# Optimization experiments

Measured on AMD Instinct MI355X. Metric: run time of the kernel, lower is better.

Reference implementation:

```python
import jax, jax.numpy as jnp
import numpy as np

EPS = 1e-5  # torch BatchNorm1d / LayerNorm default eps
B, S, CTX, C, H = 64, 31, 2048, 512, 8  # S must be num_particles+1 = 31
DH = C // H


def layernorm(x, g, b):
    mu = x.mean(-1, keepdims=True)
    var = x.var(-1, keepdims=True)
    return (x - mu) / jnp.sqrt(var + EPS) * g + b


def setup_inputs() -> dict:
    key = jax.random.key(0)
    ks = jax.random.split(key, 16)
    w = lambda k, shape: jax.random.normal(k, shape, jnp.float32) * 0.02
    return {
        "queries": jax.random.normal(ks[0], (B, S, C), jnp.float32),
        "contexts": jax.random.normal(ks[1], (B, CTX, C), jnp.float32),
        # SelfAttention params (BatchNorm1d(C) in training mode, q/k/v no bias, out with bias)
        "sa_bn_g": jnp.ones((C,), jnp.float32),
        "sa_bn_b": jnp.zeros((C,), jnp.float32),
        "sa_q_w": w(ks[2], (C, C)),
        "sa_k_w": w(ks[3], (C, C)),
        "sa_v_w": w(ks[4], (C, C)),
        "sa_out_w": w(ks[5], (C, C)),
        "sa_out_b": jnp.zeros((C,), jnp.float32),
        "sa_pre_g": jnp.ones((S * S,), jnp.float32),  # BatchNorm1d(961) on energy
        "sa_pre_b": jnp.zeros((S * S,), jnp.float32),
        # Cross Attention params (LayerNorm on queries, q/k/v no bias, out with bias)
        "ca_ln_g": jnp.ones((C,), jnp.float32),
        "ca_ln_b": jnp.zeros((C,), jnp.float32),
        "ca_q_w": w(ks[6], (C, C)),
        "ca_k_w": w(ks[7], (C, C)),
        "ca_v_w": w(ks[8], (C, C)),
        "ca_out_w": w(ks[9], (C, C)),
        "ca_out_b": jnp.zeros((C,), jnp.float32),
        # FFN: LN -> SiLU -> Linear(C,2C,no bias) -> LN -> SiLU -> Linear(2C,C,no bias)
        "ff_ln1_g": jnp.ones((C,), jnp.float32),
        "ff_ln1_b": jnp.zeros((C,), jnp.float32),
        "ff_w1": w(ks[10], (2 * C, C)),
        "ff_ln2_g": jnp.ones((2 * C,), jnp.float32),
        "ff_ln2_b": jnp.zeros((2 * C,), jnp.float32),
        "ff_w2": w(ks[11], (C, 2 * C)),
    }


def reference(queries, contexts, sa_bn_g, sa_bn_b, sa_q_w, sa_k_w, sa_v_w,
              sa_out_w, sa_out_b, sa_pre_g, sa_pre_b, ca_ln_g, ca_ln_b,
              ca_q_w, ca_k_w, ca_v_w, ca_out_w, ca_out_b, ff_ln1_g, ff_ln1_b,
              ff_w1, ff_ln2_g, ff_ln2_b, ff_w2):
    scale = jnp.sqrt(jnp.asarray(C, queries.dtype))

    # ---- SelfAttention (normalization='Batch', training-mode batch stats) ----
    mu = queries.mean(axis=(0, 1))            # per-channel over (B, S)
    var = queries.var(axis=(0, 1))
    xn = (queries - mu) / jnp.sqrt(var + EPS) * sa_bn_g + sa_bn_b
    q = jnp.einsum('bsc,oc->bso', xn, sa_q_w).reshape(B, S, H, DH)
    k = jnp.einsum('bsc,oc->bso', xn, sa_k_w).reshape(B, S, H, DH)
    v = jnp.einsum('bsc,oc->bso', xn, sa_v_w).reshape(B, S, H, DH)
    energy = jnp.einsum('nqhc,nkhc->nhqk', q, k)          # (B,H,S,S)
    # pre-softmax BatchNorm1d over channels = flattened (q,k) positions, batch dims = (B, H)
    e = energy.reshape(B, H, S * S)                        # (B,H,S*S)
    mu2 = e.mean(axis=(0, 1))
    var2 = e.var(axis=(0, 1))
    en = (e - mu2) / jnp.sqrt(var2 + EPS) * sa_pre_g + sa_pre_b
    energy_post = en.reshape(B, H, S, S)
    attn = jax.nn.softmax(energy_post / scale, axis=-1)
    o = jnp.einsum('nhql,nlhc->nqhc', attn, v).reshape(B, S, C)
    o = jnp.einsum('bsc,oc->bso', o, sa_out_w) + sa_out_b
    x_sa = o + queries                                     # residual

    # ---- Cross Attention (LayerNorm on queries pre-projection) ----
    qn = layernorm(x_sa, ca_ln_g, ca_ln_b)
    q2 = jnp.einsum('bsc,oc->bso', qn, ca_q_w).reshape(B, S, H, DH)
    k2 = jnp.einsum('btc,oc->bto', contexts, ca_k_w).reshape(B, CTX, H, DH)
    v2 = jnp.einsum('btc,oc->bto', contexts, ca_v_w).reshape(B, CTX, H, DH)
    energy2 = jnp.einsum('nqhc,nkhc->nhqk', q2, k2)        # (B,H,S,CTX)
    attn2 = jax.nn.softmax(energy2 / scale, axis=-1)
    o2 = jnp.einsum('nhql,nlhc->nqhc', attn2, v2).reshape(B, S, C)
    o2 = jnp.einsum('bsc,oc->bso', o2, ca_out_w) + ca_out_b
    x_ca = o2 + x_sa                                       # residual (queries_pre)

    # ---- FFN: LN -> SiLU -> Linear -> LN -> SiLU -> Linear, + residual ----
    h = jax.nn.silu(layernorm(x_ca, ff_ln1_g, ff_ln1_b))
    h = jnp.einsum('bsc,oc->bso', h, ff_w1)                # (B,S,2C)
    h = jax.nn.silu(layernorm(h, ff_ln2_g, ff_ln2_b))
    h = jnp.einsum('bsc,oc->bso', h, ff_w2)                # (B,S,C)
    out = x_ca + h                                         # dropout p=0.0 -> identity
    return out, energy2
```

## Files before the change

kernel.cpp:

```cpp
#include <hip/hip_runtime.h>
#include <hip/hip_bf16.h>
#include <cstdint>
#include <cstddef>

using u16 = unsigned short;
typedef short short8 __attribute__((ext_vector_type(8)));
typedef short short4v __attribute__((ext_vector_type(4)));
typedef float f32x4  __attribute__((ext_vector_type(4)));

#define DEV static __device__ __forceinline__

DEV float b2f(u16 u){ union{ unsigned i; float f; } v; v.i = ((unsigned)u)<<16; return v.f; }
DEV u16 f2b(float f){
  unsigned i = __builtin_bit_cast(unsigned, f);
  unsigned r = (i + 0x7FFFu + ((i>>16)&1u)) >> 16;
  return (u16)r;
}
DEV f32x4 mfma16(short8 a, short8 b, f32x4 c){
  return __builtin_amdgcn_mfma_f32_16x16x32_bf16(a, b, c, 0, 0, 0);
}

constexpr int Bn=64, Sn=31, Tn=2048, Cn=512, Hn=8;
constexpr int Rn=Bn*Sn;
constexpr int BHn=Bn*Hn;
constexpr int HRn=Hn*Sn;
constexpr float EPSf=1e-5f;
constexpr float INV_SCALE=0.04419417382415922f;

__global__ void k_badorder(float* out){
  if(threadIdx.x==0) out[0]=2000.f;
}

struct Src8 { const float* p[8]; };
__global__ __launch_bounds__(256) void k_cvtbn(Src8 s, u16* __restrict__ dst,
    const float* __restrict__ q, float* __restrict__ ps, float* __restrict__ psq){
  int bid=blockIdx.x;
  if(bid<1280){
    int i = bid*256 + threadIdx.x;
    int seg, j=i;
    if(j>=196608){ if(j>=262144){seg=7;j-=262144;} else {seg=6;j-=196608;} }
    else { seg=j>>15; j&=32767; }
    const float* src=s.p[seg];
    f32x4 a=*(const f32x4*)&src[(size_t)j*8];
    f32x4 b=*(const f32x4*)&src[(size_t)j*8+4];
    short8 o;
    #pragma unroll
    for(int qq=0;qq<4;++qq){ o[qq]=(short)f2b(a[qq]); o[4+qq]=(short)f2b(b[qq]); }
    *(short8*)&dst[(size_t)i*8]=o;
  } else {
    int bb=bid-1280;
    int c = (bb&1)*256 + threadIdx.x;
    int r0 = (bb>>1)*124;
    float sum=0.f, sq=0.f;
    for(int r=r0;r<r0+124;++r){ float v=q[(size_t)r*Cn+c]; sum+=v; sq+=v*v; }
    ps [(bb>>1)*Cn+c]=sum;
    psq[(bb>>1)*Cn+c]=sq;
  }
}

__global__ __launch_bounds__(512) void k_bn1_final(const float* __restrict__ ps,
    const float* __restrict__ psq, const float* __restrict__ g,
    const float* __restrict__ b, float* __restrict__ scale, float* __restrict__ shift){
  int c = threadIdx.x;
  float s=0.f, sq=0.f;
  for(int i=0;i<16;++i){ s+=ps[i*Cn+c]; sq+=psq[i*Cn+c]; }
  float m = s/(float)Rn;
  float v = sq/(float)Rn - m*m;
  float rs = rsqrtf(v+EPSf);
  float sc = rs*g[c];
  scale[c]=sc; shift[c]=b[c]-m*sc;
}

__global__ __launch_bounds__(256) void k_qkv(
    const float* __restrict__ q, const float* __restrict__ scale,
    const float* __restrict__ shift,
    const u16* __restrict__ W0, const u16* __restrict__ W1, const u16* __restrict__ W2,
    u16* __restrict__ o0, u16* __restrict__ o1v, u16* __restrict__ o2v)
{
  __shared__ u16 As[64][72];
  __shared__ u16 Ws[64][72];
  const int z=blockIdx.z;
  const u16* W = (z==0)?W0:((z==1)?W1:W2);
  u16* out     = (z==0)?o0:((z==1)?o1v:o2v);
  const int t=threadIdx.x, w=t>>6, l=t&63;
  const int m0=blockIdx.x*64, n0=blockIdx.y*64;
  const int lr=l&15, lk=(l>>4)*8;
  f32x4 zero={0.f,0.f,0.f,0.f};
  f32x4 acc[4];
  #pragma unroll
  for(int i=0;i<4;++i) acc[i]=zero;
  const int row0=t>>3, c8=(t&7)*8;
  for(int k0=0;k0<Cn;k0+=64){
    f32x4 sc0=*(const f32x4*)&scale[k0+c8], sc1=*(const f32x4*)&scale[k0+c8+4];
    f32x4 sh0=*(const f32x4*)&shift[k0+c8], sh1=*(const f32x4*)&shift[k0+c8+4];
    f32x4 x00=*(const f32x4*)&q[(size_t)(m0+row0   )*Cn+k0+c8];
    f32x4 x01=*(const f32x4*)&q[(size_t)(m0+row0   )*Cn+k0+c8+4];
    f32x4 x10=*(const f32x4*)&q[(size_t)(m0+32+row0)*Cn+k0+c8];
    f32x4 x11=*(const f32x4*)&q[(size_t)(m0+32+row0)*Cn+k0+c8+4];
    short8 a0,a1;
    #pragma unroll
    for(int j=0;j<4;++j){
      a0[j]  =(short)f2b(fmaf(x00[j],sc0[j],sh0[j]));
      a0[4+j]=(short)f2b(fmaf(x01[j],sc1[j],sh1[j]));
      a1[j]  =(short)f2b(fmaf(x10[j],sc0[j],sh0[j]));
      a1[4+j]=(short)f2b(fmaf(x11[j],sc1[j],sh1[j]));
    }
    short8 w0=*(const short8*)&W[(size_t)(n0+row0   )*Cn + k0 + c8];
    short8 w1=*(const short8*)&W[(size_t)(n0+32+row0)*Cn + k0 + c8];
    __syncthreads();
    *(short8*)&As[row0   ][c8]=a0;
    *(short8*)&As[32+row0][c8]=a1;
    *(short8*)&Ws[row0   ][c8]=w0;
    *(short8*)&Ws[32+row0][c8]=w1;
    __syncthreads();
    #pragma unroll
    for(int ks=0;ks<64;ks+=32){
      short8 af=*(const short8*)&As[w*16+lr][ks+lk];
      #pragma unroll
      for(int nf=0;nf<4;++nf){
        short8 bf=*(const short8*)&Ws[nf*16+lr][ks+lk];
        acc[nf]=mfma16(af,bf,acc[nf]);
      }
    }
  }
  const int r0=w*16+(l>>4)*4;
  #pragma unroll
  for(int nf=0;nf<4;++nf){
    const int n=n0+nf*16+lr;
    #pragma unroll
    for(int r=0;r<4;++r){
      const int m=m0+r0+r;
      out[(size_t)m*Cn+n]=f2b(acc[nf][r]);
    }
  }
}

template<bool F32OUT, bool RES32>
__global__ __launch_bounds__(256) void k_gemm64(
    const u16* __restrict__ A, const u16* __restrict__ W,
    const float* __restrict__ bias, const void* __restrict__ res,
    void* __restrict__ outv, int M, int N, int K)
{
  __shared__ u16 As[64][72];
  __shared__ u16 Ws[64][72];
  const int t=threadIdx.x, w=t>>6, l=t&63;
  const int m0=blockIdx.x*64, n0=blockIdx.y*64;
  const int lr=l&15, lk=(l>>4)*8;
  f32x4 zero={0.f,0.f,0.f,0.f};
  f32x4 acc[4];
  #pragma unroll
  for(int i=0;i<4;++i) acc[i]=zero;
  const int row0=t>>3, c8=(t&7)*8;
  for(int k0=0;k0<K;k0+=64){
    short8 a0=*(const short8*)&A[(size_t)(m0+row0   )*K + k0 + c8];
    short8 a1=*(const short8*)&A[(size_t)(m0+32+row0)*K + k0 + c8];
    short8 w0=*(const short8*)&W[(size_t)(n0+row0   )*K + k0 + c8];
    short8 w1=*(const short8*)&W[(size_t)(n0+32+row0)*K + k0 + c8];
    __syncthreads();
    *(short8*)&As[row0   ][c8]=a0;
    *(short8*)&As[32+row0][c8]=a1;
    *(short8*)&Ws[row0   ][c8]=w0;
    *(short8*)&Ws[32+row0][c8]=w1;
    __syncthreads();
    #pragma unroll
    for(int ks=0;ks<64;ks+=32){
      short8 af=*(const short8*)&As[w*16+lr][ks+lk];
      #pragma unroll
      for(int nf=0;nf<4;++nf){
        short8 bf=*(const short8*)&Ws[nf*16+lr][ks+lk];
        acc[nf]=mfma16(af,bf,acc[nf]);
      }
    }
  }
  const int r0=w*16+(l>>4)*4;
  #pragma unroll
  for(int nf=0;nf<4;++nf){
    const int n=n0+nf*16+lr;
    float bv = bias? bias[n] : 0.f;
    #pragma unroll
    for(int r=0;r<4;++r){
      const int m=m0+r0+r;
      float vv=acc[nf][r]+bv;
      if(res){
        if(RES32) vv += ((const float*)res)[(size_t)m*N+n];
        else      vv += b2f(((const u16*)res)[(size_t)m*N+n]);
      }
      if(F32OUT) ((float*)outv)[(size_t)m*N+n]=vv;
      else       ((u16*)outv)[(size_t)m*N+n]=f2b(vv);
    }
  }
}

__global__ __launch_bounds__(64) void k_energy1(const u16* __restrict__ q,
    const u16* __restrict__ k, float* __restrict__ e1){
  __shared__ u16 qs[32][72];
  __shared__ u16 ks_[32][72];
  const int bh=blockIdx.x, b=bh>>3, h=bh&7;
  const int t=threadIdx.x, l=t;
  #pragma unroll
  for(int i=0;i<4;++i){
    int flat=i*64+t; int row=flat>>3, c8=(flat&7)*8;
    short8 zq={0,0,0,0,0,0,0,0}, zk={0,0,0,0,0,0,0,0};
    if(row<31){
      zq=*(const short8*)&q[(size_t)(b*31+row)*Cn + h*64 + c8];
      zk=*(const short8*)&k[(size_t)(b*31+row)*Cn + h*64 + c8];
    }
    *(short8*)&qs [row][c8]=zq;
    *(short8*)&ks_[row][c8]=zk;
  }
  __syncthreads();
  const int lr=l&15, lk=(l>>4)*8;
  f32x4 zero={0.f,0.f,0.f,0.f};
  f32x4 acc[2][2];
  acc[0][0]=zero; acc[0][1]=zero; acc[1][0]=zero; acc[1][1]=zero;
  #pragma unroll
  for(int ks=0;ks<64;ks+=32){
    short8 a0=*(const short8*)&qs [lr   ][ks+lk];
    short8 a1=*(const short8*)&qs [16+lr][ks+lk];
    short8 b0=*(const short8*)&ks_[lr   ][ks+lk];
    short8 b1=*(const short8*)&ks_[16+lr][ks+lk];
    acc[0][0]=mfma16(a0,b0,acc[0][0]);
    acc[0][1]=mfma16(a0,b1,acc[0][1]);
    acc[1][0]=mfma16(a1,b0,acc[1][0]);
    acc[1][1]=mfma16(a1,b1,acc[1][1]);
  }
  const int r0=(l>>4)*4;
  #pragma unroll
  for(int i=0;i<2;++i)
    #pragma unroll
    for(int j=0;j<2;++j)
      #pragma unroll
      for(int r=0;r<4;++r){
        int qi=i*16+r0+r, ki=j*16+lr;
        if(qi<31 && ki<31) e1[(size_t)bh*961 + qi*31 + ki]=acc[i][j][r];
      }
}

__global__ __launch_bounds__(256) void k_bn2_partial(const float* __restrict__ e1,
    float* __restrict__ ps, float* __restrict__ psq){
  int p=blockIdx.x*256+threadIdx.x;
  if(p>=961) return;
  int r0=blockIdx.y*64;
  float s=0.f, sq=0.f;
  for(int r=r0;r<r0+64;++r){ float v=e1[(size_t)r*961+p]; s+=v; sq+=v*v; }
  ps [blockIdx.y*961+p]=s;
  psq[blockIdx.y*961+p]=sq;
}
__global__ __launch_bounds__(1024) void k_bn2_final(const float* __restrict__ ps,
    const float* __restrict__ psq, float* __restrict__ mu2, float* __restrict__ rstd2){
  int p=threadIdx.x; if(p>=961) return;
  float s=0.f, sq=0.f;
  for(int i=0;i<8;++i){ s+=ps[i*961+p]; sq+=psq[i*961+p]; }
  float m=s/512.f, v=sq/512.f-m*m;
  mu2[p]=m; rstd2[p]=rsqrtf(v+EPSf);
}

__global__ __launch_bounds__(64) void k_smpv(const float* __restrict__ e1,
    const float* __restrict__ mu2, const float* __restrict__ rstd2,
    const float* __restrict__ g2, const float* __restrict__ bb2,
    const u16* __restrict__ v, u16* __restrict__ o1){
  __shared__ u16 at[32][40];
  __shared__ u16 vs[64][40];
  const int bh=blockIdx.x, b=bh>>3, h=bh&7;
  const int l=threadIdx.x;
  for(int kv=0;kv<31;++kv) vs[l][kv]=v[(size_t)(b*31+kv)*Cn + h*64 + l];
  vs[l][31]=0;
  if(l<31){
    const float* er=e1+(size_t)bh*961 + l*31;
    float lg[31]; float mx=-1e30f;
    #pragma unroll
    for(int kk=0;kk<31;++kk){
      int p=l*31+kk;
      float en=(er[kk]-mu2[p])*rstd2[p]*g2[p]+bb2[p];
      lg[kk]=en*INV_SCALE;
      mx=fmaxf(mx,lg[kk]);
    }
    float s=0.f;
    #pragma unroll
    for(int kk=0;kk<31;++kk){ lg[kk]=__expf(lg[kk]-mx); s+=lg[kk]; }
    float inv=1.f/s;
    #pragma unroll
    for(int kk=0;kk<31;++kk) at[l][kk]=f2b(lg[kk]*inv);
    at[l][31]=0;
  } else if(l==31){
    #pragma unroll
    for(int kk=0;kk<32;++kk) at[31][kk]=0;
  }
  __syncthreads();
  const int lr=l&15, lk=(l>>4)*8;
  f32x4 zero={0.f,0.f,0.f,0.f};
  f32x4 acc[2][4];
  #pragma unroll
  for(int i=0;i<2;++i)
    #pragma unroll
    for(int nf=0;nf<4;++nf) acc[i][nf]=zero;
  short8 a0=*(const short8*)&at[lr   ][lk];
  short8 a1=*(const short8*)&at[16+lr][lk];
  #pragma unroll
  for(int nf=0;nf<4;++nf){
    short8 bf=*(const short8*)&vs[nf*16+lr][lk];
    acc[0][nf]=mfma16(a0,bf,acc[0][nf]);
    acc[1][nf]=mfma16(a1,bf,acc[1][nf]);
  }
  const int r0=(l>>4)*4;
  #pragma unroll
  for(int i=0;i<2;++i)
    #pragma unroll
    for(int nf=0;nf<4;++nf)
      #pragma unroll
      for(int r=0;r<4;++r){
        int qi=i*16+r0+r;
        if(qi<31){
          int dh=nf*16+lr;
          o1[(size_t)(b*31+qi)*Cn + h*64 + dh]=f2b(acc[i][nf][r]);
        }
      }
}

template<int Wd, bool SILU>
__global__ __launch_bounds__(256) void k_ln(const u16* __restrict__ x,
    const float* __restrict__ g, const float* __restrict__ b, u16* __restrict__ out){
  const int w=threadIdx.x>>6, l=threadIdx.x&63;
  const int row=blockIdx.x*4+w;
  constexpr int NC=Wd/512;
  float v[NC*8];
  #pragma unroll
  for(int i=0;i<NC;++i){
    short8 s=*(const short8*)&x[(size_t)row*Wd + i*512 + l*8];
    #pragma unroll
    for(int j=0;j<8;++j) v[i*8+j]=b2f((u16)s[j]);
  }
  float s1=0.f, s2=0.f;
  #pragma unroll
  for(int e=0;e<NC*8;++e){ s1+=v[e]; s2+=v[e]*v[e]; }
  #pragma unroll
  for(int off=1;off<64;off<<=1){ s1+=__shfl_xor(s1,off,64); s2+=__shfl_xor(s2,off,64); }
  float m=s1/(float)Wd, var=s2/(float)Wd-m*m, rs=rsqrtf(var+EPSf);
  #pragma unroll
  for(int i=0;i<NC;++i){
    short8 o;
    #pragma unroll
    for(int j=0;j<8;++j){
      int c=i*512+l*8+j;
      float y=(v[i*8+j]-m)*rs*g[c]+b[c];
      if(SILU) y=y/(1.f+__expf(-y));
      o[j]=(short)f2b(y);
    }
    *(short8*)&out[(size_t)row*Wd + i*512 + l*8]=o;
  }
}

__global__ __launch_bounds__(256) void k_qk(const u16* __restrict__ q2,
    const float* __restrict__ Wk, u16* __restrict__ qk){
  __shared__ u16 qs[32][72];
  __shared__ u16 bt[128][72];
  const int bh=blockIdx.x, b=bh>>3, h=bh&7;
  const int t=threadIdx.x, w=t>>6, l=t&63;
  {
    int row=t>>3, c8=(t&7)*8;
    short8 z={0,0,0,0,0,0,0,0};
    if(row<31) z=*(const short8*)&q2[(size_t)(b*31+row)*Cn + h*64 + c8];
    *(short8*)&qs[row][c8]=z;
  }
  const int lr=l&15, lk=(l>>4)*8;
  const int r0=(l>>4)*4;
  for(int nc=0;nc<512;nc+=128){
    __syncthreads();
    #pragma unroll
    for(int i=0;i<8;++i){
      int g=i*256+t;
      int d=g>>5, c4=(g&31)*4;
      f32x4 v=*(const f32x4*)&Wk[(size_t)(h*64+d)*Cn + nc + c4];
      #pragma unroll
      for(int jj=0;jj<4;++jj) bt[c4+jj][d]=f2b(v[jj]);
    }
    __syncthreads();
    f32x4 zero={0.f,0.f,0.f,0.f};
    f32x4 acc[2][2];
    acc[0][0]=zero; acc[0][1]=zero; acc[1][0]=zero; acc[1][1]=zero;
    #pragma unroll
    for(int ks=0;ks<64;ks+=32){
      short8 a0=*(const short8*)&qs[lr   ][ks+lk];
      short8 a1=*(const short8*)&qs[16+lr][ks+lk];
      #pragma unroll
      for(int nf=0;nf<2;++nf){
        short8 bf=*(const short8*)&bt[w*32+nf*16+lr][ks+lk];
        acc[0][nf]=mfma16(a0,bf,acc[0][nf]);
        acc[1][nf]=mfma16(a1,bf,acc[1][nf]);
      }
    }
    #pragma unroll
    for(int i=0;i<2;++i)
      #pragma unroll
      for(int nf=0;nf<2;++nf)
        #pragma unroll
        for(int r=0;r<4;++r){
          int qi=i*16+r0+r;
          if(qi<31)
            qk[((size_t)b*HRn + h*31 + qi)*Cn + nc + w*32 + nf*16 + lr]=f2b(acc[i][nf][r]);
        }
  }
}

__global__ __launch_bounds__(512) void k_e2big(const u16* __restrict__ qk,
    const float* __restrict__ ctx, float* __restrict__ e2, u16* __restrict__ ctxb){
  __shared__ u16 As[256][72];
  __shared__ u16 Bs[128][72];
  const int tb=blockIdx.x*128, b=blockIdx.y;
  const int t=threadIdx.x, w=t>>6, l=t&63;
  const int lr=l&15, lk=(l>>4)*8;
  const int wr=(w>>1)*64, wc=(w&1)*64;
  f32x4 zero={0.f,0.f,0.f,0.f};
  f32x4 acc[4][4];
  #pragma unroll
  for(int i=0;i<4;++i)
    #pragma unroll
    for(int j=0;j<4;++j) acc[i][j]=zero;
  for(int k0=0;k0<512;k0+=64){
    __syncthreads();
    #pragma unroll
    for(int i=0;i<4;++i){
      int g=i*512+t; int row=g>>3, c8=(g&7)*8;
      short8 z={0,0,0,0,0,0,0,0};
      if(row<HRn) z=*(const short8*)&qk[((size_t)b*HRn+row)*Cn + k0 + c8];
      *(short8*)&As[row][c8]=z;
    }
    #pragma unroll
    for(int i=0;i<4;++i){
      int g=i*512+t; int row=g>>4, c4=(g&15)*4;
      f32x4 v=*(const f32x4*)&ctx[((size_t)b*Tn + tb + row)*Cn + k0 + c4];
      short4v o;
      #pragma unroll
      for(int jj=0;jj<4;++jj) o[jj]=(short)f2b(v[jj]);
      *(short4v*)&Bs[row][c4]=o;
      __builtin_nontemporal_store(o,
        (short4v*)&ctxb[((size_t)b*Tn + tb + row)*Cn + k0 + c4]);
    }
    __syncthreads();
    #pragma unroll
    for(int ks=0;ks<64;ks+=32){
      short8 af[4], bf[4];
      #pragma unroll
      for(int i=0;i<4;++i){
        af[i]=*(const short8*)&As[wr+i*16+lr][ks+lk];
        bf[i]=*(const short8*)&Bs[wc+i*16+lr][ks+lk];
      }
      #pragma unroll
      for(int i=0;i<4;++i)
        #pragma unroll
        for(int j=0;j<4;++j)
          acc[i][j]=mfma16(af[i],bf[j],acc[i][j]);
    }
  }
  const int r0=(l>>4)*4;
  #pragma unroll
  for(int i=0;i<4;++i)
    #pragma unroll
    for(int j=0;j<4;++j)
      #pragma unroll
      for(int r=0;r<4;++r){
        int rm=wr+i*16+r0+r;
        if(rm<HRn)
          e2[((size_t)b*HRn+rm)*Tn + tb + wc + j*16 + lr]=acc[i][j][r];
      }
}

__global__ __launch_bounds__(256) void k_pstats(const float* __restrict__ e2,
    u16* __restrict__ pb, float* __restrict__ st){
  const int w=threadIdx.x>>6, l=threadIdx.x&63;
  const int gi=blockIdx.x*4+w;
  const int b=gi>>8, m=gi&255;
  u16* pr = pb + ((size_t)b*256+m)*2048;
  if(m>=HRn){
    short8 z={0,0,0,0,0,0,0,0};
    #pragma unroll
    for(int i=0;i<4;++i) *(short8*)&pr[i*512 + l*8]=z;
    return;
  }
  const float* er = e2 + ((size_t)b*HRn+m)*Tn;
  float v[32];
  #pragma unroll
  for(int i=0;i<4;++i){
    f32x4 a=*(const f32x4*)&er[i*512 + l*8];
    f32x4 c=*(const f32x4*)&er[i*512 + l*8 + 4];
    #pragma unroll
    for(int j=0;j<4;++j){ v[i*8+j]=a[j]*INV_SCALE; v[i*8+4+j]=c[j]*INV_SCALE; }
  }
  float mx=v[0];
  #pragma unroll
  for(int e=1;e<32;++e) mx=fmaxf(mx,v[e]);
  #pragma unroll
  for(int off=1;off<64;off<<=1) mx=fmaxf(mx,__shfl_xor(mx,off,64));
  float s=0.f;
  #pragma unroll
  for(int e=0;e<32;++e){ v[e]=__expf(v[e]-mx); s+=v[e]; }
  #pragma unroll
  for(int off=1;off<64;off<<=1) s+=__shfl_xor(s,off,64);
  #pragma unroll
  for(int i=0;i<4;++i){
    short8 o;
    #pragma unroll
    for(int j=0;j<8;++j) o[j]=(short)f2b(v[i*8+j]);
    *(short8*)&pr[i*512 + l*8]=o;
  }
  if(l==0){ st[2*((size_t)b*HRn+m)]=mx; st[2*((size_t)b*HRn+m)+1]=s; }
}

__global__ __launch_bounds__(512) void k_pv2(const u16* __restrict__ pb,
    const u16* __restrict__ ctxb, const float* __restrict__ st,
    u16* __restrict__ o2t){
  __shared__ u16 As[128][72];
  __shared__ u16 Bs[128][76];
  const int n0=blockIdx.x*128, m0=blockIdx.y*128, b=blockIdx.z;
  const int t=threadIdx.x, w=t>>6, l=t&63;
  const int lr=l&15, lk=(l>>4)*8;
  const int wm=(w>>2)*64, wn=(w&3)*32;
  f32x4 zero={0.f,0.f,0.f,0.f};
  f32x4 acc[4][2];
  #pragma unroll
  for(int i=0;i<4;++i){ acc[i][0]=zero; acc[i][1]=zero; }
  const int arow=t>>3, ac8=(t&7)*8;
  const int bc2=(t&63)*2, bg=t>>6;
  for(int kb=0;kb<Tn;kb+=64){
    __syncthreads();
    #pragma unroll
    for(int i=0;i<2;++i){
      int row=arow+i*64;
      *(short8*)&As[row][ac8] =
        *(const short8*)&pb[((size_t)b*256 + m0 + row)*Tn + kb + ac8];
    }
    #pragma unroll
    for(int i=0;i<2;++i){
      int r0 = bg*8 + i*4;
      const u16* base=&ctxb[((size_t)b*Tn + kb + r0)*Cn + n0 + bc2];
      unsigned v0=*(const unsigned*)(base);
      unsigned v1=*(const unsigned*)(base + Cn);
      unsigned v2=*(const unsigned*)(base + 2*Cn);
      unsigned v3=*(const unsigned*)(base + 3*Cn);
      short4v lo={(short)(v0&0xffffu),(short)(v1&0xffffu),(short)(v2&0xffffu),(short)(v3&0xffffu)};
      short4v hi={(short)(v0>>16),(short)(v1>>16),(short)(v2>>16),(short)(v3>>16)};
      *(short4v*)&Bs[bc2  ][r0]=lo;
      *(short4v*)&Bs[bc2+1][r0]=hi;
    }
    __syncthreads();
    #pragma unroll
    for(int ks=0;ks<64;ks+=32){
      short8 af[4], bf[2];
      #pragma unroll
      for(int i=0;i<4;++i)
        af[i]=*(const short8*)&As[wm+i*16+lr][ks+lk];
      #pragma unroll
      for(int j=0;j<2;++j){
        const u16* p=&Bs[wn+j*16+lr][ks+lk];
        short4v lo=*(const short4v*)p;
        short4v hi=*(const short4v*)(p+4);
        short8 bb;
        #pragma unroll
        for(int jj=0;jj<4;++jj){ bb[jj]=lo[jj]; bb[4+jj]=hi[jj]; }
        bf[j]=bb;
      }
      #pragma unroll
      for(int i=0;i<4;++i)
        #pragma unroll
        for(int j=0;j<2;++j)
          acc[i][j]=mfma16(af[i],bf[j],acc[i][j]);
    }
  }
  const int r0=(l>>4)*4;
  #pragma unroll
  for(int i=0;i<4;++i)
    #pragma unroll
    for(int j=0;j<2;++j)
      #pragma unroll
      for(int r=0;r<4;++r){
        int rm=m0+wm+i*16+r0+r;
        if(rm<HRn){
          float inv=1.f/st[2*((size_t)b*HRn+rm)+1];
          o2t[((size_t)b*HRn+rm)*Cn + n0+wn+j*16+lr]=f2b(acc[i][j][r]*inv);
        }
      }
}

__global__ __launch_bounds__(256) void k_o2proj(const u16* __restrict__ o2t,
    const float* __restrict__ Wv, u16* __restrict__ o2b){
  __shared__ u16 As[32][72];
  __shared__ u16 Ws[64][72];
  const int bh=blockIdx.x, b=bh>>3, h=bh&7;
  const int t=threadIdx.x, w=t>>6, l=t&63;
  const int lr=l&15, lk=(l>>4)*8;
  f32x4 zero={0.f,0.f,0.f,0.f};
  f32x4 acc[2]; acc[0]=zero; acc[1]=zero;
  for(int k0=0;k0<512;k0+=64){
    __syncthreads();
    {
      int row=t>>3, c8=(t&7)*8;
      short8 z={0,0,0,0,0,0,0,0};
      if(row<31) z=*(const short8*)&o2t[((size_t)b*HRn + h*31 + row)*Cn + k0 + c8];
      *(short8*)&As[row][c8]=z;
    }
    #pragma unroll
    for(int i=0;i<4;++i){
      int g=i*256+t; int row=g>>4, c4=(g&15)*4;
      f32x4 v=*(const f32x4*)&Wv[(size_t)(h*64+row)*Cn + k0 + c4];
      short4v o;
      #pragma unroll
      for(int jj=0;jj<4;++jj) o[jj]=(short)f2b(v[jj]);
      *(short4v*)&Ws[row][c4]=o;
    }
    __syncthreads();
    #pragma unroll
    for(int ks=0;ks<64;ks+=32){
      short8 a0=*(const short8*)&As[lr   ][ks+lk];
      short8 a1=*(const short8*)&As[16+lr][ks+lk];
      short8 bf=*(const short8*)&Ws[w*16+lr][ks+lk];
      acc[0]=mfma16(a0,bf,acc[0]);
      acc[1]=mfma16(a1,bf,acc[1]);
    }
  }
  const int r0=(l>>4)*4;
  #pragma unroll
  for(int i=0;i<2;++i)
    #pragma unroll
    for(int r=0;r<4;++r){
      int qi=i*16+r0+r;
      if(qi<31)
        o2b[((size_t)b*31+qi)*Cn + h*64 + w*16 + lr]=f2b(acc[i][r]);
    }
}

extern "C" void kernel_launch(void* const* d_in, const int* in_sizes, int n_in,
                              void* d_out, int out_size, void* d_ws, size_t ws_size,
                              hipStream_t stream){
  (void)out_size; (void)ws_size;
  float* outp=(float*)d_out;
  float* e2  =outp + (size_t)Rn*Cn;
  if(n_in<24 || in_sizes[0]!=Rn*Cn || in_sizes[1]!=Bn*Tn*Cn ||
     in_sizes[4]!=Cn*Cn || in_sizes[9]!=961 || in_sizes[20]!=2*Cn*Cn){
    k_badorder<<<1,64,0,stream>>>(outp);
    return;
  }
  const float* queries =(const float*)d_in[0];
  const float* contexts=(const float*)d_in[1];
  const float* sa_bn_g =(const float*)d_in[2];
  const float* sa_bn_b =(const float*)d_in[3];
  const float* sa_q_w  =(const float*)d_in[4];
  const float* sa_k_w  =(const float*)d_in[5];
  const float* sa_v_w  =(const float*)d_in[6];
  const float* sa_out_w=(const float*)d_in[7];
  const float* sa_out_b=(const float*)d_in[8];
  const float* sa_pre_g=(const float*)d_in[9];
  const float* sa_pre_b=(const float*)d_in[10];
  const float* ca_ln_g =(const float*)d_in[11];
  const float* ca_ln_b =(const float*)d_in[12];
  const float* ca_q_w  =(const float*)d_in[13];
  const float* ca_k_w  =(const float*)d_in[14];
  const float* ca_v_w  =(const float*)d_in[15];
  const float* ca_out_w=(const float*)d_in[16];
  const float* ca_out_b=(const float*)d_in[17];
  const float* ff_ln1_g=(const float*)d_in[18];
  const float* ff_ln1_b=(const float*)d_in[19];
  const float* ff_w1   =(const float*)d_in[20];
  const float* ff_ln2_g=(const float*)d_in[21];
  const float* ff_ln2_b=(const float*)d_in[22];
  const float* ff_w2   =(const float*)d_in[23];

  char* ws=(char*)d_ws;
  size_t off=0;
  auto alloc=[&](size_t bytes)->char*{
    char* p=ws+off; off=(off+bytes+255)&~(size_t)255; return p;
  };
  float* ps1  =(float*)alloc(16*Cn*4);
  float* psq1 =(float*)alloc(16*Cn*4);
  float* scale1=(float*)alloc(Cn*4);
  float* shift1=(float*)alloc(Cn*4);
  u16* w_sq=(u16*)alloc((size_t)Cn*Cn*2);
  u16* w_sk=(u16*)alloc((size_t)Cn*Cn*2);
  u16* w_sv=(u16*)alloc((size_t)Cn*Cn*2);
  u16* w_so=(u16*)alloc((size_t)Cn*Cn*2);
  u16* w_cq=(u16*)alloc((size_t)Cn*Cn*2);
  u16* w_co=(u16*)alloc((size_t)Cn*Cn*2);
  u16* w_f1=(u16*)alloc((size_t)2*Cn*Cn*2);
  u16* w_f2=(u16*)alloc((size_t)2*Cn*Cn*2);
  u16* qb  =(u16*)alloc((size_t)Rn*Cn*2);
  u16* kb  =(u16*)alloc((size_t)Rn*Cn*2);
  u16* vb  =(u16*)alloc((size_t)Rn*Cn*2);
  float* e1  =(float*)alloc((size_t)BHn*961*4);
  float* ps2 =(float*)alloc(8*961*4);
  float* psq2=(float*)alloc(8*961*4);
  float* mu2 =(float*)alloc(961*4);
  float* rstd2=(float*)alloc(961*4);
  u16* o1  =(u16*)alloc((size_t)Rn*Cn*2);
  u16* xsa =(u16*)alloc((size_t)Rn*Cn*2);
  u16* qn  =(u16*)alloc((size_t)Rn*Cn*2);
  u16* q2b =(u16*)alloc((size_t)Rn*Cn*2);
  u16* qk  =(u16*)alloc((size_t)Bn*HRn*Cn*2);
  float* st=(float*)alloc((size_t)BHn*31*2*4);
  u16* o2b =(u16*)alloc((size_t)Rn*Cn*2);
  u16* xca =(u16*)alloc((size_t)Rn*Cn*2);
  u16* pb  =(u16*)alloc((size_t)Bn*256*Tn*2);
  u16* ctxb=(u16*)alloc((size_t)Bn*Tn*Cn*2);
  u16* o2t = qk;
  u16* f1  = o1;
  u16* t1  = qb;
  u16* f2  = vb;

  dim3 blk256(256), blk64(64), blk512(512);
  dim3 g64(Rn/64, Cn/64);

  Src8 s8; s8.p[0]=sa_q_w; s8.p[1]=sa_k_w; s8.p[2]=sa_v_w; s8.p[3]=sa_out_w;
  s8.p[4]=ca_q_w; s8.p[5]=ca_out_w; s8.p[6]=ff_w1; s8.p[7]=ff_w2;
  k_cvtbn<<<1312,blk256,0,stream>>>(s8, w_sq, queries, ps1, psq1);

  k_bn1_final<<<1,512,0,stream>>>(ps1,psq1,sa_bn_g,sa_bn_b,scale1,shift1);
  k_qkv<<<dim3(31,8,3),blk256,0,stream>>>(queries,scale1,shift1,w_sq,w_sk,w_sv,qb,kb,vb);
  k_energy1<<<BHn,blk64,0,stream>>>(qb,kb,e1);
  k_bn2_partial<<<dim3(4,8),blk256,0,stream>>>(e1,ps2,psq2);
  k_bn2_final<<<1,1024,0,stream>>>(ps2,psq2,mu2,rstd2);
  k_smpv<<<BHn,blk64,0,stream>>>(e1,mu2,rstd2,sa_pre_g,sa_pre_b,vb,o1);
  k_gemm64<false,true><<<g64,blk256,0,stream>>>(o1,w_so,sa_out_b,queries,xsa,Rn,Cn,Cn);

  k_ln<512,false><<<Rn/4,blk256,0,stream>>>(xsa,ca_ln_g,ca_ln_b,qn);
  k_gemm64<false,false><<<g64,blk256,0,stream>>>(qn,w_cq,nullptr,nullptr,q2b,Rn,Cn,Cn);
  k_qk<<<BHn,blk256,0,stream>>>(q2b,ca_k_w,qk);
  k_e2big<<<dim3(Tn/128,Bn),blk512,0,stream>>>(qk,contexts,e2,ctxb);
  k_pstats<<<Bn*256/4,blk256,0,stream>>>(e2,pb,st);
  k_pv2<<<dim3(Cn/128,2,Bn),blk512,0,stream>>>(pb,ctxb,st,o2t);
  k_o2proj<<<BHn,blk256,0,stream>>>(o2t,ca_v_w,o2b);
  k_gemm64<false,false><<<g64,blk256,0,stream>>>(o2b,w_co,ca_out_b,xsa,xca,Rn,Cn,Cn);

  k_ln<512,true><<<Rn/4,blk256,0,stream>>>(xca,ff_ln1_g,ff_ln1_b,f1);
  k_gemm64<false,false><<<dim3(Rn/64,1024/64),blk256,0,stream>>>(f1,w_f1,nullptr,nullptr,t1,Rn,1024,Cn);
  k_ln<1024,true><<<Rn/4,blk256,0,stream>>>(t1,ff_ln2_g,ff_ln2_b,f2);
  k_gemm64<true,false><<<g64,blk256,0,stream>>>(f2,w_f2,nullptr,xca,outp,Rn,Cn,1024);
}
```

Before: 440.2 us.

## Prefetch next K-tile into registers in e2big and pv2 GEMM loops

Both the cross-attention energy GEMM and the PV GEMM now load the next K-tile from global memory into registers while the MFMA loop runs on the current shared-memory tile. This is software pipelining meant to hide global load latency behind compute. The PV kernel also changes its ctxb gather from 32-bit paired loads to per-element 16-bit loads. The ctxb store in e2big drops its nontemporal hint. The added prefetch registers raise register pressure, and the narrower loads in pv2 may reduce memory efficiency.

```diff
diff --git a/kernel.cpp b/kernel.cpp
--- a/kernel.cpp
+++ b/kernel.cpp
@@ -416,27 +416,38 @@
   for(int i=0;i<4;++i)
     #pragma unroll
     for(int j=0;j<4;++j) acc[i][j]=zero;
+
+  const int arow[4]={ (0*512+t)>>3, (1*512+t)>>3, (2*512+t)>>3, (3*512+t)>>3 };
+  const int ac8=(t&7)*8;
+  const int brow=t>>4, bc4=(t&15)*4;
+  short8 areg[4];
+  f32x4  breg[4];
+  auto loadK=[&](int k0){
+    #pragma unroll
+    for(int i=0;i<4;++i){
+      short8 z={0,0,0,0,0,0,0,0};
+      if(arow[i]<HRn) z=*(const short8*)&qk[((size_t)b*HRn+arow[i])*Cn + k0 + ac8];
+      areg[i]=z;
+    }
+    #pragma unroll
+    for(int i=0;i<4;++i)
+      breg[i]=*(const f32x4*)&ctx[((size_t)b*Tn + tb + i*32+brow)*Cn + k0 + bc4];
+  };
+  loadK(0);
   for(int k0=0;k0<512;k0+=64){
     __syncthreads();
     #pragma unroll
+    for(int i=0;i<4;++i) *(short8*)&As[arow[i]][ac8]=areg[i];
+    #pragma unroll
     for(int i=0;i<4;++i){
-      int g=i*512+t; int row=g>>3, c8=(g&7)*8;
-      short8 z={0,0,0,0,0,0,0,0};
-      if(row<HRn) z=*(const short8*)&qk[((size_t)b*HRn+row)*Cn + k0 + c8];
-      *(short8*)&As[row][c8]=z;
-    }
-    #pragma unroll
-    for(int i=0;i<4;++i){
-      int g=i*512+t; int row=g>>4, c4=(g&15)*4;
-      f32x4 v=*(const f32x4*)&ctx[((size_t)b*Tn + tb + row)*Cn + k0 + c4];
       short4v o;
       #pragma unroll
-      for(int jj=0;jj<4;++jj) o[jj]=(short)f2b(v[jj]);
-      *(short4v*)&Bs[row][c4]=o;
-      __builtin_nontemporal_store(o,
-        (short4v*)&ctxb[((size_t)b*Tn + tb + row)*Cn + k0 + c4]);
-    }
-    __syncthreads();
+      for(int jj=0;jj<4;++jj) o[jj]=(short)f2b(breg[i][jj]);
+      *(short4v*)&Bs[i*32+brow][bc4]=o;
+      *(short4v*)&ctxb[((size_t)b*Tn + tb + i*32+brow)*Cn + k0 + bc4]=o;
+    }
+    __syncthreads();
+    if(k0+64<512) loadK(k0+64);
     #pragma unroll
     for(int ks=0;ks<64;ks+=32){
       short8 af[4], bf[4];
@@ -520,29 +531,35 @@
   #pragma unroll
   for(int i=0;i<4;++i){ acc[i][0]=zero; acc[i][1]=zero; }
   const int arow=t>>3, ac8=(t&7)*8;
-  const int bc2=(t&63)*2, bg=t>>6;
+  const int bc=t&127, bq=(t>>7)*4;
+  short8 areg[2];
+  u16 breg[16];
+  auto loadK=[&](int kb){
+    #pragma unroll
+    for(int i=0;i<2;++i)
+      areg[i]=*(const short8*)&pb[((size_t)b*256 + m0 + arow+i*64)*Tn + kb + ac8];
+    #pragma unroll
+    for(int i=0;i<4;++i){
+      int kt0=(bq+i)*4;
+      #pragma unroll
+      for(int jj=0;jj<4;++jj)
+        breg[i*4+jj]=ctxb[((size_t)b*Tn + kb + kt0 + jj)*Cn + n0 + bc];
+    }
+  };
+  loadK(0);
   for(int kb=0;kb<Tn;kb+=64){
     __syncthreads();
     #pragma unroll
-    for(int i=0;i<2;++i){
-      int row=arow+i*64;
-      *(short8*)&As[row][ac8] =
-        *(const short8*)&pb[((size_t)b*256 + m0 + row)*Tn + kb + ac8];
-    }
-    #pragma unroll
-    for(int i=0;i<2;++i){
-      int r0 = bg*8 + i*4;
-      const u16* base=&ctxb[((size_t)b*Tn + kb + r0)*Cn + n0 + bc2];
-      unsigned v0=*(const unsigned*)(base);
-      unsigned v1=*(const unsigned*)(base + Cn);
-      unsigned v2=*(const unsigned*)(base + 2*Cn);
-      unsigned v3=*(const unsigned*)(base + 3*Cn);
-      short4v lo={(short)(v0&0xffffu),(short)(v1&0xffffu),(short)(v2&0xffffu),(short)(v3&0xffffu)};
-      short4v hi={(short)(v0>>16),(short)(v1>>16),(short)(v2>>16),(short)(v3>>16)};
-      *(short4v*)&Bs[bc2  ][r0]=lo;
-      *(short4v*)&Bs[bc2+1][r0]=hi;
-    }
-    __syncthreads();
+    for(int i=0;i<2;++i) *(short8*)&As[arow+i*64][ac8]=areg[i];
+    #pragma unroll
+    for(int i=0;i<4;++i){
+      short4v o;
+      #pragma unroll
+      for(int jj=0;jj<4;++jj) o[jj]=(short)breg[i*4+jj];
+      *(short4v*)&Bs[bc][(bq+i)*4]=o;
+    }
+    __syncthreads();
+    if(kb+64<Tn) loadK(kb+64);
     #pragma unroll
     for(int ks=0;ks<64;ks+=32){
       short8 af[4], bf[2];
```

Result: faster. 424.2 us (-3.6%).
